# Kernel tuning notes

Hardware: AMD Instinct MI355X
Metric: run time of the kernel (lower is better)

Reference implementation:

```python
import jax, jax.numpy as jnp
import numpy as np

TRANSLATION_SCALE = 1.0
ROTATION_SCALE = 0.1
EPS = 1e-05


def setup_inputs() -> dict:
    key = jax.random.key(0)
    uv = jax.random.normal(key, (2000000, 3), dtype=jnp.float32)
    return {"uv": uv}


def reference(uv):
    # uv: [B, 3] = [x, y, p_yaw]
    B = uv.shape[0]
    w = uv[:, 2] * ROTATION_SCALE                     # omega_z, [B]
    theta_sqr = w * w
    theta = jnp.sqrt(theta_sqr)                       # = |w|
    A = jnp.sin(theta) / (theta + EPS)                # sin(theta)/theta
    Bc = (1.0 - jnp.cos(theta)) / (theta_sqr + EPS)   # (1-cos)/theta^2
    C = (1.0 - A) / (theta_sqr + EPS)                 # (1-A)/theta^2

    # skew(w) for z-only rotation: [[0,-w,0],[w,0,0],[0,0,0]]
    zeros = jnp.zeros_like(w)
    skew = jnp.stack([
        jnp.stack([zeros, -w, zeros], axis=-1),
        jnp.stack([w, zeros, zeros], axis=-1),
        jnp.stack([zeros, zeros, zeros], axis=-1),
    ], axis=-2)                                        # [B,3,3]
    # skew @ skew = diag(-w^2, -w^2, 0)
    skew2 = jnp.stack([
        jnp.stack([-theta_sqr, zeros, zeros], axis=-1),
        jnp.stack([zeros, -theta_sqr, zeros], axis=-1),
        jnp.stack([zeros, zeros, zeros], axis=-1),
    ], axis=-2)                                        # [B,3,3]

    I3 = jnp.eye(3, dtype=uv.dtype)
    R = I3 + A[:, None, None] * skew + Bc[:, None, None] * skew2   # rotation [B,3,3]
    V = I3 + Bc[:, None, None] * skew + C[:, None, None] * skew2   # left-Jacobian-like [B,3,3]

    u = jnp.stack([uv[:, 0] * TRANSLATION_SCALE,
                   uv[:, 1] * TRANSLATION_SCALE,
                   zeros], axis=-1)                    # [B,3]
    t = jnp.einsum('bij,bj->bi', V, u)                 # translation [B,3]

    top = jnp.concatenate([R, t[:, :, None]], axis=-1) # [B,3,4]
    bottom = jnp.broadcast_to(jnp.array([0., 0., 0., 1.], dtype=uv.dtype), (B, 1, 4))
    return jnp.concatenate([top, bottom], axis=-2)     # [B,4,4]
```

## Files before the change

### kernel.cpp

```cpp
#include <hip/hip_runtime.h>


#define ROTATION_SCALE 0.1f
#define EPS_F 1e-5f

__global__ __launch_bounds__(256) void lie_se3_kernel(
    const float* __restrict__ uv, float4* __restrict__ out, int B) {
  __shared__ float4 smem[1024];

  int tid = threadIdx.x;
  int m = blockIdx.x * 256 + tid;

  float x = 0.0f, y = 0.0f, p = 0.0f;
  if (m < B) {
    x = uv[3 * m + 0];
    y = uv[3 * m + 1];
    p = uv[3 * m + 2];
  }

  float w = p * ROTATION_SCALE;
  float ts = w * w;
  float th = fabsf(w);
  float s = __sinf(th);
  float c = __cosf(th);
  float A  = s / (th + EPS_F);
  float Bc = (1.0f - c) / (ts + EPS_F);
  float C  = (1.0f - A) / (ts + EPS_F);

  float R00 = 1.0f - Bc * ts;
  float Aw  = A * w;
  float V00 = 1.0f - C * ts;
  float Bw  = Bc * w;
  float t0 = V00 * x - Bw * y;
  float t1 = Bw * x + V00 * y;

  smem[4 * tid + 0] = make_float4(R00, -Aw, 0.0f, t0);
  smem[4 * tid + 1] = make_float4(Aw, R00, 0.0f, t1);
  smem[4 * tid + 2] = make_float4(0.0f, 0.0f, 1.0f, 0.0f);
  smem[4 * tid + 3] = make_float4(0.0f, 0.0f, 0.0f, 1.0f);
  __syncthreads();

  long long base = (long long)blockIdx.x * 1024;
  long long limit = 4LL * B;
  #pragma unroll
  for (int k = 0; k < 4; ++k) {
    int idx = tid + k * 256;
    long long g = base + idx;
    if (g < limit) out[g] = smem[idx];
  }
}

extern "C" void kernel_launch(void* const* d_in, const int* in_sizes, int n_in,
                              void* d_out, int out_size, void* d_ws, size_t ws_size,
                              hipStream_t stream) {
  const float* uv = (const float*)d_in[0];
  float4* out = (float4*)d_out;
  int B = in_sizes[0] / 3;
  int block = 256;
  int grid = (B + block - 1) / block;
  lie_se3_kernel<<<grid, block, 0, stream>>>(uv, out, B);
}
```

Measured before the change: 140.3 us.

## Stage input through LDS with float4 loads and use nontemporal output stores

Each block now loads its 768-float slice of the input with 192 coalesced float4 loads into shared memory, and each thread then reads its own x, y, yaw triple from there. Before, every thread did three strided scalar loads. Output stores become nontemporal stores to avoid cache pollution on the large write stream. This adds one more barrier. The tail assumes in_sizes is a multiple of 4, otherwise the last float4 is dropped.

```diff
diff --git a/kernel.cpp b/kernel.cpp
--- a/kernel.cpp
+++ b/kernel.cpp
@@ -4,19 +4,27 @@
 #define ROTATION_SCALE 0.1f
 #define EPS_F 1e-5f
 
+typedef float nfloat4 __attribute__((ext_vector_type(4)));
+
 __global__ __launch_bounds__(256) void lie_se3_kernel(
-    const float* __restrict__ uv, float4* __restrict__ out, int B) {
-  __shared__ float4 smem[1024];
+    const float4* __restrict__ uv4, float4* __restrict__ out,
+    int B, int n4in) {
+  __shared__ float sin_buf[768];
+  __shared__ float4 sout[1024];
 
   int tid = threadIdx.x;
-  int m = blockIdx.x * 256 + tid;
+  int blk = blockIdx.x;
 
-  float x = 0.0f, y = 0.0f, p = 0.0f;
-  if (m < B) {
-    x = uv[3 * m + 0];
-    y = uv[3 * m + 1];
-    p = uv[3 * m + 2];
+  if (tid < 192) {
+    int g4 = blk * 192 + tid;
+    float4 v = (g4 < n4in) ? uv4[g4] : make_float4(0.f, 0.f, 0.f, 0.f);
+    ((float4*)sin_buf)[tid] = v;
   }
+  __syncthreads();
+
+  float x = sin_buf[3 * tid + 0];
+  float y = sin_buf[3 * tid + 1];
+  float p = sin_buf[3 * tid + 2];
 
   float w = p * ROTATION_SCALE;
   float ts = w * w;
@@ -34,29 +42,35 @@
   float t0 = V00 * x - Bw * y;
   float t1 = Bw * x + V00 * y;
 
-  smem[4 * tid + 0] = make_float4(R00, -Aw, 0.0f, t0);
-  smem[4 * tid + 1] = make_float4(Aw, R00, 0.0f, t1);
-  smem[4 * tid + 2] = make_float4(0.0f, 0.0f, 1.0f, 0.0f);
-  smem[4 * tid + 3] = make_float4(0.0f, 0.0f, 0.0f, 1.0f);
+  sout[4 * tid + 0] = make_float4(R00, -Aw, 0.0f, t0);
+  sout[4 * tid + 1] = make_float4(Aw, R00, 0.0f, t1);
+  sout[4 * tid + 2] = make_float4(0.0f, 0.0f, 1.0f, 0.0f);
+  sout[4 * tid + 3] = make_float4(0.0f, 0.0f, 0.0f, 1.0f);
   __syncthreads();
 
-  long long base = (long long)blockIdx.x * 1024;
+  long long base = (long long)blk * 1024;
   long long limit = 4LL * B;
+  nfloat4* outN = (nfloat4*)out;
+  const nfloat4* soutN = (const nfloat4*)sout;
   #pragma unroll
   for (int k = 0; k < 4; ++k) {
     int idx = tid + k * 256;
     long long g = base + idx;
-    if (g < limit) out[g] = smem[idx];
+    if (g < limit) {
+      nfloat4 v = soutN[idx];
+      __builtin_nontemporal_store(v, &outN[g]);
+    }
   }
 }
 
 extern "C" void kernel_launch(void* const* d_in, const int* in_sizes, int n_in,
                               void* d_out, int out_size, void* d_ws, size_t ws_size,
                               hipStream_t stream) {
-  const float* uv = (const float*)d_in[0];
+  const float4* uv4 = (const float4*)d_in[0];
   float4* out = (float4*)d_out;
   int B = in_sizes[0] / 3;
+  int n4in = in_sizes[0] / 4;
   int block = 256;
   int grid = (B + block - 1) / block;
-  lie_se3_kernel<<<grid, block, 0, stream>>>(uv, out, B);
+  lie_se3_kernel<<<grid, block, 0, stream>>>(uv4, out, B, n4in);
 }
```

Measured after the change: 147.3 us. 5.0% more time.
